# Optimization experiments

Hardware: AMD Instinct MI355X
Metric: run time of the kernel (lower is better)

## Reference

```python
import jax, jax.numpy as jnp
import numpy as np

B, S, E, H, Dh = 2, 2048, 1024, 16, 64


def setup_inputs() -> dict:
    key = jax.random.key(0)
    ks = jax.random.split(key, 8)
    w = 0.02
    return {
        "x": jax.random.normal(ks[0], (B, S, E), jnp.float32),
        # torch Linear convention: weight (out, in) = (Dh, E), stacked over heads
        "Wq": jax.random.normal(ks[1], (H, Dh, E), jnp.float32) * w,
        "bq": jax.random.normal(ks[2], (H, Dh), jnp.float32) * w,
        "Wk": jax.random.normal(ks[3], (H, Dh, E), jnp.float32) * w,
        "bk": jax.random.normal(ks[4], (H, Dh), jnp.float32) * w,
        "Wv": jax.random.normal(ks[5], (H, Dh, E), jnp.float32) * w,
        "bv": jax.random.normal(ks[6], (H, Dh), jnp.float32) * w,
        "proj": jax.random.normal(ks[7], (H * Dh, E), jnp.float32) * w,
    }


def reference(x, Wq, bq, Wk, bk, Wv, bv, proj):
    b, s, e = x.shape
    h, dh, _ = Wq.shape
    scale = jnp.sqrt(jnp.asarray(dh, x.dtype))
    # per-head linear projections: y = x @ W.T + b  -> (b, h, s, dh)
    q = jnp.einsum('bse,hde->bhsd', x, Wq) + bq[None, :, None, :]
    k = jnp.einsum('bse,hde->bhsd', x, Wk) + bk[None, :, None, :]
    v = jnp.einsum('bse,hde->bhsd', x, Wv) + bv[None, :, None, :]
    causal = jnp.triu(jnp.ones((s, s), bool), 1)
    scores = jnp.einsum('bhsd,bhtd->bhst', q, k) / scale
    scores = jnp.where(causal[None, None], -jnp.inf, scores)
    # quirk: softmax output divided by sqrt(head_size) a second time
    att = jax.nn.softmax(scores, axis=-1) / scale
    z = jnp.einsum('bhst,bhtd->bhsd', att, v)
    # quirk: torch reshapes (B,H,S,Dh) row-major into (B,S,H*Dh) WITHOUT transpose
    z = z.reshape(b, s, h * dh)
    return z @ proj
```

## Files before the change

kernel.cpp:

```cpp
#include <hip/hip_runtime.h>
#include <hip/hip_bf16.h>

typedef unsigned short u16;
typedef unsigned int u32;
typedef __bf16 bf16x8 __attribute__((ext_vector_type(8)));
typedef float f32x4 __attribute__((ext_vector_type(4)));
typedef u16 u16x8 __attribute__((ext_vector_type(8)));
typedef u16 u16x4 __attribute__((ext_vector_type(4)));
typedef u32 u32x4 __attribute__((ext_vector_type(4)));

#define B_ 2
#define S_ 2048
#define E_ 1024
#define H_ 16
#define Dh_ 64

static __device__ __forceinline__ u16 f2bf(float f) {
  unsigned u = __builtin_bit_cast(unsigned, f);
  u += 0x7fff + ((u >> 16) & 1);
  return (u16)(u >> 16);
}

static __device__ __forceinline__ void gload16(const u16* g, u16* l) {
  __builtin_amdgcn_global_load_lds((const __attribute__((address_space(1))) unsigned int*)g,
                                   (__attribute__((address_space(3))) unsigned int*)l,
                                   16, 0, 0);
}

__global__ void cvt_all(const float* __restrict__ x, const float* __restrict__ wq,
                        const float* __restrict__ wk, const float* __restrict__ wv,
                        const float* __restrict__ proj,
                        u16* __restrict__ xb, u16* __restrict__ wcat, u16* __restrict__ pjt) {
  __shared__ float tt[32][33];
  const int bid = blockIdx.x;
  const int tid = threadIdx.x;
  if (bid < 3584) {
    const int i = bid * 256 + tid;
    const float* src; u16x8* dst;
    if (i < 524288) {
      src = x + (size_t)i * 8;            dst = (u16x8*)xb + i;
    } else {
      const int j = i - 524288;
      dst = (u16x8*)wcat + j;
      if (j < 131072)      src = wq + (size_t)j * 8;
      else if (j < 262144) src = wk + (size_t)(j - 131072) * 8;
      else                 src = wv + (size_t)(j - 262144) * 8;
    }
    float4 a = ((const float4*)src)[0], b = ((const float4*)src)[1];
    u16x8 o;
    o[0] = f2bf(a.x); o[1] = f2bf(a.y); o[2] = f2bf(a.z); o[3] = f2bf(a.w);
    o[4] = f2bf(b.x); o[5] = f2bf(b.y); o[6] = f2bf(b.z); o[7] = f2bf(b.w);
    *dst = o;
  } else {
    const int tb = bid - 3584;
    const int e0 = (tb & 31) * 32, f0 = (tb >> 5) * 32;
    const int tx = tid & 31, ty = tid >> 5;
#pragma unroll
    for (int r = 0; r < 4; ++r) {
      const int row = ty + r * 8;
      tt[row][tx] = proj[(f0 + row) * 1024 + e0 + tx];
    }
    __syncthreads();
#pragma unroll
    for (int r = 0; r < 4; ++r) {
      const int row = ty + r * 8;
      pjt[(e0 + row) * 1024 + f0 + tx] = f2bf(tt[tx][row]);
    }
  }
}

__global__ __launch_bounds__(512, 2) void qkv_gemm(const u16* __restrict__ Wcat,
                                                   const u16* __restrict__ Xm,
                                                   const float* __restrict__ bq,
                                                   const float* __restrict__ bk,
                                                   const float* __restrict__ bv,
                                                   u16* __restrict__ Qb, u16* __restrict__ Kb,
                                                   u16* __restrict__ Vtb, float qs) {
  __shared__ __align__(16) u16 Alds[2][12288];
  __shared__ __align__(16) u16 Blds[2][16384];
  const int tid = threadIdx.x;
  const int wv = tid >> 6, ln = tid & 63;
  const int lq = ln & 15, lg = ln >> 4;
  const int wm = wv >> 2, wn = wv & 3;
  const int bid = blockIdx.x;
  const int xcd = bid & 7, w = bid >> 3;
  const int bx = w & 15;
  const int by = xcd * 2 + (w >> 4);
  const int ra0 = bx * 192, rb0 = by * 256;

  const int r_t = tid >> 3, c_t = tid & 7;
  const int gcol = (c_t ^ (r_t & 7)) * 8;
  const u16* Asrc = Wcat + (ra0 + r_t) * 1024 + gcol;
  const u16* Bsrc = Xm   + (rb0 + r_t) * 1024 + gcol;

  const int sc0 = (lg ^ (lq & 7)) * 8;
  const int sc1 = ((4 + lg) ^ (lq & 7)) * 8;
  const int baseA = (wm * 96 + lq) * 64;
  const int baseB = (wn * 64 + lq) * 64;

  f32x4 acc[6][4];
  const f32x4 z4 = {0.f, 0.f, 0.f, 0.f};
#pragma unroll
  for (int i = 0; i < 6; ++i)
#pragma unroll
    for (int j = 0; j < 4; ++j) acc[i][j] = z4;

#define SA(G, KT, BUF) gload16(Asrc + (G) * 65536 + (KT) * 64, &Alds[BUF][((G) * 512 + tid) * 8])
#define SB(G, KT, BUF) gload16(Bsrc + (G) * 65536 + (KT) * 64, &Blds[BUF][((G) * 512 + tid) * 8])
#define LOADA(MH, SC) do {                                                         \
    _Pragma("unroll") for (int ii = 0; ii < 3; ++ii)                               \
      af[ii] = *(const bf16x8*)&Alds[cb][baseA + (MH) * 3072 + ii * 1024 + (SC)];  \
  } while (0)
#define LOADB(DST, SC) do {                                                        \
    _Pragma("unroll") for (int j = 0; j < 4; ++j)                                  \
      DST[j] = *(const bf16x8*)&Blds[cb][baseB + j * 1024 + (SC)];                 \
  } while (0)
#define MF(MH, BQ) do {                                                            \
    _Pragma("unroll") for (int ii = 0; ii < 3; ++ii)                               \
      _Pragma("unroll") for (int j = 0; j < 4; ++j)                                \
        acc[(MH) * 3 + ii][j] =                                                    \
            __builtin_amdgcn_mfma_f32_16x16x32_bf16(af[ii], BQ[j],                 \
                                                    acc[(MH) * 3 + ii][j], 0, 0, 0); \
  } while (0)

  SB(0, 0, 0); SB(1, 0, 0); SB(2, 0, 0); SB(3, 0, 0);
  SA(0, 0, 0); SA(1, 0, 0); SA(2, 0, 0);

  for (int kt = 0; kt < 16; ++kt) {
    const int cb = kt & 1, nb = cb ^ 1;
    const bool st = (kt < 15);
    asm volatile("s_waitcnt vmcnt(0)" ::: "memory");
    __builtin_amdgcn_s_barrier();
    __builtin_amdgcn_sched_barrier(0);
    bf16x8 af[3], bq0[4], bq1[4];
    LOADA(0, sc0);
    LOADB(bq0, sc0);
    if (st) { SB(0, kt + 1, nb); SB(1, kt + 1, nb); }
    __builtin_amdgcn_s_barrier();
    asm volatile("s_waitcnt lgkmcnt(0)" ::: "memory");
    __builtin_amdgcn_sched_barrier(0);
    __builtin_amdgcn_s_setprio(1);
    MF(0, bq0);
    __builtin_amdgcn_s_setprio(0);
    __builtin_amdgcn_s_barrier();
    LOADA(0, sc1);
    LOADB(bq1, sc1);
    if (st) { SB(2, kt + 1, nb); SB(3, kt + 1, nb); }
    __builtin_amdgcn_s_barrier();
    asm volatile("s_waitcnt lgkmcnt(0)" ::: "memory");
    __builtin_amdgcn_sched_barrier(0);
    __builtin_amdgcn_s_setprio(1);
    MF(0, bq1);
    __builtin_amdgcn_s_setprio(0);
    __builtin_amdgcn_s_barrier();
    LOADA(1, sc0);
    if (st) { SA(0, kt + 1, nb); SA(1, kt + 1, nb); }
    __builtin_amdgcn_s_barrier();
    asm volatile("s_waitcnt lgkmcnt(0)" ::: "memory");
    __builtin_amdgcn_sched_barrier(0);
    __builtin_amdgcn_s_setprio(1);
    MF(1, bq0);
    __builtin_amdgcn_s_setprio(0);
    __builtin_amdgcn_s_barrier();
    LOADA(1, sc1);
    if (st) { SA(2, kt + 1, nb); }
    __builtin_amdgcn_s_barrier();
    asm volatile("s_waitcnt lgkmcnt(0)" ::: "memory");
    __builtin_amdgcn_sched_barrier(0);
    __builtin_amdgcn_s_setprio(1);
    MF(1, bq1);
    __builtin_amdgcn_s_setprio(0);
    __builtin_amdgcn_s_barrier();
  }
#undef SA
#undef SB
#undef LOADA
#undef LOADB
#undef MF

#pragma unroll
  for (int i = 0; i < 6; ++i) {
    const int n0 = ra0 + wm * 96 + i * 16 + lg * 4;
    const int reg_i = n0 >> 10;
    const int nl = n0 & 1023;
    const int h = nl >> 6, d = nl & 63;
    const float* bias = (reg_i == 0) ? bq : (reg_i == 1) ? bk : bv;
    const float osc = (reg_i == 0) ? qs : 1.0f;
    const float4 b4 = *(const float4*)&bias[nl];
#pragma unroll
    for (int j = 0; j < 4; ++j) {
      const int m = rb0 + wn * 64 + j * 16 + lq;
      const int bb = m >> 11, s = m & 2047;
      if (reg_i < 2) {
        u16* out = (reg_i == 0) ? Qb : Kb;
        u16x4 pk;
        pk[0] = f2bf((acc[i][j][0] + b4.x) * osc);
        pk[1] = f2bf((acc[i][j][1] + b4.y) * osc);
        pk[2] = f2bf((acc[i][j][2] + b4.z) * osc);
        pk[3] = f2bf((acc[i][j][3] + b4.w) * osc);
        *(u16x4*)&out[((bb * H_ + h) * S_ + s) * Dh_ + d] = pk;
      } else {
        const float bvv[4] = {b4.x, b4.y, b4.z, b4.w};
#pragma unroll
        for (int r = 0; r < 4; ++r)
          Vtb[((bb * H_ + h) * Dh_ + d + r) * S_ + s] = f2bf(acc[i][j][r] + bvv[r]);
      }
    }
  }
}

__global__ __launch_bounds__(256) void proj_gemm(const u16* __restrict__ Am,
                                                 const u16* __restrict__ Bm,
                                                 float* __restrict__ out) {
  __shared__ __align__(16) u16 As[2][4096];
  __shared__ __align__(16) u16 Bs[2][2048];
  const int tid = threadIdx.x;
  const int wv = tid >> 6, ln = tid & 63;
  const int lq = ln & 15, lg = ln >> 4;
  const int bid = blockIdx.x;
  const int xcd = bid & 7, within = bid >> 3;
  const int bx = within & 7;
  const int by = xcd * 8 + (within >> 3);
  const int ra0 = bx * 128, rb0 = by * 64;
  const int wra = wv >> 1, wrb = wv & 1;

  f32x4 acc[4][2];
  const f32x4 z4 = {0.f, 0.f, 0.f, 0.f};
#pragma unroll
  for (int i = 0; i < 4; ++i)
#pragma unroll
    for (int j = 0; j < 2; ++j) acc[i][j] = z4;

  const int arow = tid >> 2;
  const int acol = (tid & 3) * 8;
  const int brow = wv * 16 + (ln >> 2);
  const int bcol = (ln & 3) * 8;
  const u16* Ags = Am + (ra0 + arow) * 1024 + acol;
  const u16* Bgs = Bm + (rb0 + brow) * 1024 + bcol;

#define PSTAGE(KT, BUF) do { const int k0_ = (KT) * 32;              \
    gload16(Ags + k0_,         &As[BUF][wv * 512]);                  \
    gload16(Ags + 65536 + k0_, &As[BUF][wv * 512 + 2048]);           \
    gload16(Bgs + k0_,         &Bs[BUF][wv * 512]); } while (0)

  PSTAGE(0, 0);
  for (int kt = 0; kt < 32; ++kt) {
    const int cb = kt & 1;
    asm volatile("s_waitcnt vmcnt(0)" ::: "memory");
    __builtin_amdgcn_s_barrier();
    __builtin_amdgcn_sched_barrier(0);
    if (kt < 31) PSTAGE(kt + 1, cb ^ 1);
    bf16x8 af[4], bfr[2];
#pragma unroll
    for (int i = 0; i < 4; ++i)
      af[i] = *(const bf16x8*)&As[cb][(wra * 64 + i * 16 + lq) * 32 + lg * 8];
#pragma unroll
    for (int j = 0; j < 2; ++j)
      bfr[j] = *(const bf16x8*)&Bs[cb][(wrb * 32 + j * 16 + lq) * 32 + lg * 8];
    __builtin_amdgcn_s_setprio(1);
#pragma unroll
    for (int i = 0; i < 4; ++i)
#pragma unroll
      for (int j = 0; j < 2; ++j)
        acc[i][j] = __builtin_amdgcn_mfma_f32_16x16x32_bf16(af[i], bfr[j], acc[i][j], 0, 0, 0);
    __builtin_amdgcn_s_setprio(0);
  }
#undef PSTAGE

  const int Ar = ra0 + wra * 64, Br = rb0 + wrb * 32;
#pragma unroll
  for (int i = 0; i < 4; ++i)
#pragma unroll
    for (int j = 0; j < 2; ++j) {
      const int e0 = Ar + i * 16 + lg * 4;
      const int m = Br + j * 16 + lq;
      *(f32x4*)&out[m * 1024 + e0] = acc[i][j];
    }
}

__global__ __launch_bounds__(512, 4) void attn_kernel(const u16* __restrict__ Q,
                                                      const u16* __restrict__ K,
                                                      const u16* __restrict__ Vt,
                                                      u16* __restrict__ Z) {
  __shared__ __align__(16) u16 Ktile[2][8192];
  __shared__ __align__(16) u16 Vtile[2][8192];
  const int tid = threadIdx.x;
  const int wv = tid >> 6, ln = tid & 63;
  const int lq = ln & 15, lg = ln >> 4;
  const bool lgodd = (lg & 1) != 0;
  const int id = blockIdx.x;
  const int within = id >> 3;
  const int xg = id & 7;
  int bh, qt;
  if (within < 32) { bh = xg * 4 + (within >> 4);     qt = 15 - (within & 15); }
  else { const int w = within - 32; bh = xg * 4 + 2 + (w >> 4); qt = w & 15; }
  const int qrow = (qt << 7) + wv * 16 + lq;
  const u16* Qp = Q + (size_t)bh * S_ * Dh_;
  const u16* Kp = K + (size_t)bh * S_ * Dh_;
  const u16* Vp = Vt + (size_t)bh * Dh_ * S_;

  int kgofs[2], vgrow[2], vgcol[2];
#pragma unroll
  for (int j = 0; j < 2; ++j) {
    const int p = j * 512 + tid;
    const int gk = p ^ ((p >> 3) & 7);
    kgofs[j] = (gk >> 3) * 64 + (gk & 7) * 8;
    vgrow[j] = p >> 4;
    vgcol[j] = ((p & 15) ^ ((p >> 4) & 15)) * 8;
  }
  const int sc0 = (lg ^ (lq & 7)) * 8;
  const int sc1 = ((4 + lg) ^ (lq & 7)) * 8;

  bf16x8 qf0 = *(const bf16x8*)&Qp[qrow * Dh_ + lg * 8];
  bf16x8 qf1 = *(const bf16x8*)&Qp[qrow * Dh_ + 32 + lg * 8];

  f32x4 o[4];
  const f32x4 z4 = {0.f, 0.f, 0.f, 0.f};
#pragma unroll
  for (int dt = 0; dt < 4; ++dt) o[dt] = z4;
  float l_lane = 0.f;

#define STAGE(KT, BUF) do { const int kb_ = (KT) * 128;                              \
    gload16(Kp + (size_t)kb_ * 64 + kgofs[0], &Ktile[BUF][wv * 512]);                \
    gload16(Kp + (size_t)kb_ * 64 + kgofs[1], &Ktile[BUF][4096 + wv * 512]);         \
    gload16(Vp + (size_t)vgrow[0] * 2048 + kb_ + vgcol[0], &Vtile[BUF][wv * 512]);   \
    gload16(Vp + (size_t)vgrow[1] * 2048 + kb_ + vgcol[1], &Vtile[BUF][4096 + wv * 512]); \
  } while (0)

  STAGE(0, 0);

  int cur = 0;
  for (int kt = 0; kt <= qt; ++kt) {
    asm volatile("s_waitcnt vmcnt(0)" ::: "memory");
    __builtin_amdgcn_s_barrier();
    __builtin_amdgcn_sched_barrier(0);
    if (kt < qt) STAGE(kt + 1, cur ^ 1);
    const int k0 = kt * 128;
    const bool diag = (kt == qt);
    const int nkk = diag ? ((wv >> 1) + 1) : 4;

    f32x4 sa[4], sb[4];
    __builtin_amdgcn_s_setprio(1);
#pragma unroll
    for (int kk = 0; kk < 4; ++kk) {
      if (kk < nkk) {
        const int rA = (kk * 32 + lq) * 64;
        const int rB = rA + 1024;
        bf16x8 kA0 = *(const bf16x8*)&Ktile[cur][rA + sc0];
        bf16x8 kA1 = *(const bf16x8*)&Ktile[cur][rA + sc1];
        bf16x8 kB0 = *(const bf16x8*)&Ktile[cur][rB + sc0];
        bf16x8 kB1 = *(const bf16x8*)&Ktile[cur][rB + sc1];
        f32x4 a = z4, b = z4;
        a = __builtin_amdgcn_mfma_f32_16x16x32_bf16(kA0, qf0, a, 0, 0, 0);
        a = __builtin_amdgcn_mfma_f32_16x16x32_bf16(kA1, qf1, a, 0, 0, 0);
        b = __builtin_amdgcn_mfma_f32_16x16x32_bf16(kB0, qf0, b, 0, 0, 0);
        b = __builtin_amdgcn_mfma_f32_16x16x32_bf16(kB1, qf1, b, 0, 0, 0);
        sa[kk] = a; sb[kk] = b;
      }
    }
    __builtin_amdgcn_s_setprio(0);

#pragma unroll
    for (int kk = 0; kk < 4; ++kk) {
      if (kk < nkk) {
        f32x4 xa = sa[kk], xb = sb[kk];
        if (diag) {
          const int keyA = k0 + kk * 32 + lg * 4;
          const int keyB = keyA + 16;
#pragma unroll
          for (int r = 0; r < 4; ++r) {
            if (keyA + r > qrow) xa[r] = -3.0e38f;
            if (keyB + r > qrow) xb[r] = -3.0e38f;
          }
        }
        float e0 = __builtin_amdgcn_exp2f(xa[0]);
        float e1 = __builtin_amdgcn_exp2f(xa[1]);
        float e2 = __builtin_amdgcn_exp2f(xa[2]);
        float e3 = __builtin_amdgcn_exp2f(xa[3]);
        float f0 = __builtin_amdgcn_exp2f(xb[0]);
        float f1 = __builtin_amdgcn_exp2f(xb[1]);
        float f2 = __builtin_amdgcn_exp2f(xb[2]);
        float f3 = __builtin_amdgcn_exp2f(xb[3]);
        l_lane += ((e0 + e1) + (e2 + e3)) + ((f0 + f1) + (f2 + f3));
        u32 A0, A1, B0, B1;
        asm("v_cvt_pk_bf16_f32 %0, %1, %2" : "=v"(A0) : "v"(e0), "v"(e1));
        asm("v_cvt_pk_bf16_f32 %0, %1, %2" : "=v"(A1) : "v"(e2), "v"(e3));
        asm("v_cvt_pk_bf16_f32 %0, %1, %2" : "=v"(B0) : "v"(f0), "v"(f1));
        asm("v_cvt_pk_bf16_f32 %0, %1, %2" : "=v"(B1) : "v"(f2), "v"(f3));
        asm("v_permlane32_swap_b32 %0, %1" : "+v"(A0), "+v"(B0));
        asm("v_permlane32_swap_b32 %0, %1" : "+v"(A1), "+v"(B1));
        const u32 A0x = __shfl_xor((int)A0, 16), B0x = __shfl_xor((int)B0, 16);
        const u32 A1x = __shfl_xor((int)A1, 16), B1x = __shfl_xor((int)B1, 16);
        u32x4 w;
        w[0] = lgodd ? B0x : A0;
        w[1] = lgodd ? B1x : A1;
        w[2] = lgodd ? B0 : A0x;
        w[3] = lgodd ? B1 : A1x;
        const bf16x8 pf = __builtin_bit_cast(bf16x8, w);
        const int scvk = ((kk * 4 + lg) ^ lq) * 8;
        __builtin_amdgcn_s_setprio(1);
#pragma unroll
        for (int dt = 0; dt < 4; ++dt) {
          bf16x8 vf = *(const bf16x8*)&Vtile[cur][(dt * 16 + lq) * 128 + scvk];
          o[dt] = __builtin_amdgcn_mfma_f32_16x16x32_bf16(vf, pf, o[dt], 0, 0, 0);
        }
        __builtin_amdgcn_s_setprio(0);
      }
    }
    cur ^= 1;
  }
#undef STAGE

  float l = l_lane;
  l += __shfl_xor(l, 16);
  l += __shfl_xor(l, 32);
  const float inv = 0.125f / l;
#pragma unroll
  for (int dt = 0; dt < 4; ++dt) {
    u16x4 pko;
#pragma unroll
    for (int r = 0; r < 4; ++r) pko[r] = f2bf(o[dt][r] * inv);
    *(u16x4*)&Z[((size_t)bh * S_ + qrow) * Dh_ + dt * 16 + lg * 4] = pko;
  }
}

extern "C" void kernel_launch(void* const* d_in, const int* in_sizes, int n_in,
                              void* d_out, int out_size, void* d_ws, size_t ws_size,
                              hipStream_t stream) {
  const float* x    = (const float*)d_in[0];
  const float* Wq   = (const float*)d_in[1];
  const float* bq   = (const float*)d_in[2];
  const float* Wk   = (const float*)d_in[3];
  const float* bk   = (const float*)d_in[4];
  const float* Wv   = (const float*)d_in[5];
  const float* bv   = (const float*)d_in[6];
  const float* proj = (const float*)d_in[7];
  float* out = (float*)d_out;

  char* p = (char*)d_ws;
  u16* xb   = (u16*)p; p += (size_t)4096 * 1024 * 2;
  u16* wcat = (u16*)p; p += (size_t)3072 * 1024 * 2;
  u16* pjt  = (u16*)p; p += (size_t)1024 * 1024 * 2;
  u16* Qb   = (u16*)p; p += (size_t)4096 * 1024 * 2;
  u16* Kb   = (u16*)p; p += (size_t)4096 * 1024 * 2;
  u16* Vtb  = (u16*)p; p += (size_t)4096 * 1024 * 2;
  u16* Zb   = (u16*)p; p += (size_t)4096 * 1024 * 2;

  cvt_all<<<dim3(4608), dim3(256), 0, stream>>>(x, Wq, Wk, Wv, proj, xb, wcat, pjt);

  const float qs = 0.125f * 1.44269504f;
  qkv_gemm<<<dim3(256), dim3(512), 0, stream>>>(wcat, xb, bq, bk, bv, Qb, Kb, Vtb, qs);

  attn_kernel<<<dim3(512), dim3(512), 0, stream>>>(Qb, Kb, Vtb, Zb);

  proj_gemm<<<dim3(512), dim3(256), 0, stream>>>(pjt, Zb, out);
}
```

Before: 98.67 us.

## Rework projection GEMM into 128x128 tiles with 8 waves, K=64 steps, swizzled LDS

The output projection GEMM moves from 128x64 tiles with 4 waves to 128x128 tiles with 8 waves. Each K step now covers 64 elements, and the LDS layout is XOR-swizzled to avoid bank conflicts. Global loads for the next stage are split into A and B halves and interleaved between two MFMA phases, separated by extra barriers. The goal is more operand reuse per block and fewer loop iterations, at the cost of more barriers, more LDS per block, and half as many blocks (256).

Result: no change. 97.70 us (-1.0%).

```diff
diff --git a/kernel.cpp b/kernel.cpp
--- a/kernel.cpp
+++ b/kernel.cpp
@@ -209,20 +209,30 @@
   }
 }
 
-__global__ __launch_bounds__(256) void proj_gemm(const u16* __restrict__ Am,
-                                                 const u16* __restrict__ Bm,
-                                                 float* __restrict__ out) {
-  __shared__ __align__(16) u16 As[2][4096];
-  __shared__ __align__(16) u16 Bs[2][2048];
+__global__ __launch_bounds__(512, 2) void proj_gemm(const u16* __restrict__ Am,
+                                                    const u16* __restrict__ Bm,
+                                                    float* __restrict__ out) {
+  __shared__ __align__(16) u16 Alds[2][8192];
+  __shared__ __align__(16) u16 Blds[2][8192];
   const int tid = threadIdx.x;
   const int wv = tid >> 6, ln = tid & 63;
   const int lq = ln & 15, lg = ln >> 4;
+  const int wm = wv >> 2, wn = wv & 3;
   const int bid = blockIdx.x;
-  const int xcd = bid & 7, within = bid >> 3;
-  const int bx = within & 7;
-  const int by = xcd * 8 + (within >> 3);
-  const int ra0 = bx * 128, rb0 = by * 64;
-  const int wra = wv >> 1, wrb = wv & 1;
+  const int xcd = bid & 7, w = bid >> 3;
+  const int bx = w & 7;
+  const int by = xcd * 4 + (w >> 3);
+  const int ra0 = bx * 128, rb0 = by * 128;
+
+  const int r_t = tid >> 3, c_t = tid & 7;
+  const int gcol = (c_t ^ (r_t & 7)) * 8;
+  const u16* Asrc = Am + (ra0 + r_t) * 1024 + gcol;
+  const u16* Bsrc = Bm + (rb0 + r_t) * 1024 + gcol;
+
+  const int sc0 = (lg ^ (lq & 7)) * 8;
+  const int sc1 = ((4 + lg) ^ (lq & 7)) * 8;
+  const int baseA = (wm * 64 + lq) * 64;
+  const int baseB = (wn * 32 + lq) * 64;
 
   f32x4 acc[4][2];
   const f32x4 z4 = {0.f, 0.f, 0.f, 0.f};
@@ -231,49 +241,60 @@
 #pragma unroll
     for (int j = 0; j < 2; ++j) acc[i][j] = z4;
 
-  const int arow = tid >> 2;
-  const int acol = (tid & 3) * 8;
-  const int brow = wv * 16 + (ln >> 2);
-  const int bcol = (ln & 3) * 8;
-  const u16* Ags = Am + (ra0 + arow) * 1024 + acol;
-  const u16* Bgs = Bm + (rb0 + brow) * 1024 + bcol;
-
-#define PSTAGE(KT, BUF) do { const int k0_ = (KT) * 32;              \
-    gload16(Ags + k0_,         &As[BUF][wv * 512]);                  \
-    gload16(Ags + 65536 + k0_, &As[BUF][wv * 512 + 2048]);           \
-    gload16(Bgs + k0_,         &Bs[BUF][wv * 512]); } while (0)
-
-  PSTAGE(0, 0);
-  for (int kt = 0; kt < 32; ++kt) {
-    const int cb = kt & 1;
+#define SA(G, KT, BUF) gload16(Asrc + (G) * 65536 + (KT) * 64, &Alds[BUF][((G) * 512 + tid) * 8])
+#define SB(G, KT, BUF) gload16(Bsrc + (G) * 65536 + (KT) * 64, &Blds[BUF][((G) * 512 + tid) * 8])
+#define LOADAB(SC) do {                                                            \
+    _Pragma("unroll") for (int ii = 0; ii < 4; ++ii)                               \
+      af[ii] = *(const bf16x8*)&Alds[cb][baseA + ii * 1024 + (SC)];                \
+    _Pragma("unroll") for (int j = 0; j < 2; ++j)                                  \
+      bf[j] = *(const bf16x8*)&Blds[cb][baseB + j * 1024 + (SC)];                  \
+  } while (0)
+#define MF() do {                                                                  \
+    _Pragma("unroll") for (int ii = 0; ii < 4; ++ii)                               \
+      _Pragma("unroll") for (int j = 0; j < 2; ++j)                                \
+        acc[ii][j] = __builtin_amdgcn_mfma_f32_16x16x32_bf16(af[ii], bf[j],        \
+                                                             acc[ii][j], 0, 0, 0); \
+  } while (0)
+
+  SA(0, 0, 0); SA(1, 0, 0); SB(0, 0, 0); SB(1, 0, 0);
+
+  for (int kt = 0; kt < 16; ++kt) {
+    const int cb = kt & 1, nb = cb ^ 1;
+    const bool st = (kt < 15);
     asm volatile("s_waitcnt vmcnt(0)" ::: "memory");
     __builtin_amdgcn_s_barrier();
     __builtin_amdgcn_sched_barrier(0);
-    if (kt < 31) PSTAGE(kt + 1, cb ^ 1);
-    bf16x8 af[4], bfr[2];
-#pragma unroll
-    for (int i = 0; i < 4; ++i)
-      af[i] = *(const bf16x8*)&As[cb][(wra * 64 + i * 16 + lq) * 32 + lg * 8];
-#pragma unroll
-    for (int j = 0; j < 2; ++j)
-      bfr[j] = *(const bf16x8*)&Bs[cb][(wrb * 32 + j * 16 + lq) * 32 + lg * 8];
-    __builtin_amdgcn_s_setprio(1);
-#pragma unroll
-    for (int i = 0; i < 4; ++i)
-#pragma unroll
-      for (int j = 0; j < 2; ++j)
-        acc[i][j] = __builtin_amdgcn_mfma_f32_16x16x32_bf16(af[i], bfr[j], acc[i][j], 0, 0, 0);
-    __builtin_amdgcn_s_setprio(0);
-  }
-#undef PSTAGE
-
-  const int Ar = ra0 + wra * 64, Br = rb0 + wrb * 32;
+    bf16x8 af[4], bf[2];
+    LOADAB(sc0);
+    if (st) { SA(0, kt + 1, nb); SA(1, kt + 1, nb); }
+    __builtin_amdgcn_s_barrier();
+    asm volatile("s_waitcnt lgkmcnt(0)" ::: "memory");
+    __builtin_amdgcn_sched_barrier(0);
+    __builtin_amdgcn_s_setprio(1);
+    MF();
+    __builtin_amdgcn_s_setprio(0);
+    __builtin_amdgcn_s_barrier();
+    LOADAB(sc1);
+    if (st) { SB(0, kt + 1, nb); SB(1, kt + 1, nb); }
+    __builtin_amdgcn_s_barrier();
+    asm volatile("s_waitcnt lgkmcnt(0)" ::: "memory");
+    __builtin_amdgcn_sched_barrier(0);
+    __builtin_amdgcn_s_setprio(1);
+    MF();
+    __builtin_amdgcn_s_setprio(0);
+    __builtin_amdgcn_s_barrier();
+  }
+#undef SA
+#undef SB
+#undef LOADAB
+#undef MF
+
 #pragma unroll
   for (int i = 0; i < 4; ++i)
 #pragma unroll
     for (int j = 0; j < 2; ++j) {
-      const int e0 = Ar + i * 16 + lg * 4;
-      const int m = Br + j * 16 + lq;
+      const int e0 = ra0 + wm * 64 + i * 16 + lg * 4;
+      const int m = rb0 + wn * 32 + j * 16 + lq;
       *(f32x4*)&out[m * 1024 + e0] = acc[i][j];
     }
 }
@@ -453,5 +474,5 @@
 
   attn_kernel<<<dim3(512), dim3(512), 0, stream>>>(Qb, Kb, Vtb, Zb);
 
-  proj_gemm<<<dim3(512), dim3(256), 0, stream>>>(pjt, Zb, out);
-}
+  proj_gemm<<<dim3(256), dim3(512), 0, stream>>>(pjt, Zb, out);
+}
```
